# Kernel optimization log

Measured on AMD Instinct MI355X. Metric: run time of the kernel, lower is better.

Reference implementation:

```python
import jax, jax.numpy as jnp
import numpy as np

B, S, E, H = 4, 2048, 1024, 16
D = E // H


def setup_inputs() -> dict:
    key = jax.random.key(0)
    ks = jax.random.split(key, 8)
    inv = 1.0 / np.sqrt(E)
    return {
        "query": jax.random.normal(ks[0], (B, S, E), dtype=jnp.float32),
        "key": jax.random.normal(ks[1], (B, S, E), dtype=jnp.float32),
        "value": jax.random.normal(ks[2], (B, S, E), dtype=jnp.float32),
        "key_padding_mask": jnp.zeros((B, S), dtype=bool),
        "Wq": jax.random.uniform(ks[3], (E, E), jnp.float32, -inv, inv),
        "Wk": jax.random.uniform(ks[4], (E, E), jnp.float32, -inv, inv),
        "Wv": jax.random.uniform(ks[5], (E, E), jnp.float32, -inv, inv),
        "Wo": jax.random.uniform(ks[6], (E, E), jnp.float32, -inv, inv),
        "gamma": jnp.ones((H,), dtype=jnp.float32),
    }


def reference(query, key, value, key_padding_mask, Wq, Wk, Wv, Wo, gamma):
    b, s, e = query.shape
    h = gamma.shape[0]
    d = e // h
    # torch Linear: x @ W.T ; split into heads -> [b, h, s, d]
    q = (query @ Wq.T).reshape(b, s, h, d).swapaxes(1, 2)
    k = (key @ Wk.T).reshape(b, key.shape[1], h, d).swapaxes(1, 2)
    v = (value @ Wv.T).reshape(b, value.shape[1], h, d).swapaxes(1, 2)
    scores = jnp.einsum("bhqd,bhkd->bhqk", q, k) / jnp.sqrt(jnp.asarray(d, q.dtype))
    scores = jnp.where(key_padding_mask[:, None, None, :], -jnp.inf, scores)
    attn = jax.nn.softmax(scores, axis=-1)  # dropout p=0 in eval-equivalent reference
    out = jnp.einsum("bhqk,bhkd->bhqd", attn, v)
    out = out * gamma[None, :, None, None]  # head-scale
    out = out.swapaxes(1, 2).reshape(b, s, e)
    return out @ Wo.T
```

## Files before the change

kernel.cpp:

```cpp
#include <hip/hip_runtime.h>
#include <hip/hip_bf16.h>
#include <cstdint>

typedef __bf16 bf16;
typedef __bf16 bf16_8 __attribute__((ext_vector_type(8)));
typedef __bf16 bf16_4 __attribute__((ext_vector_type(4)));
typedef float f32_4 __attribute__((ext_vector_type(4)));
typedef short s16x4 __attribute__((ext_vector_type(4)));

#define MFMA_16x16x32(a, b, c) __builtin_amdgcn_mfma_f32_16x16x32_bf16((a), (b), (c), 0, 0, 0)
#define MFMA_16x16x16(a, b, c) __builtin_amdgcn_mfma_f32_16x16x16bf16_1k((a), (b), (c), 0, 0, 0)

__device__ __forceinline__ void gll16(const void* g, void* l) {
  __builtin_amdgcn_global_load_lds((const __attribute__((address_space(1))) void*)g,
                                   (__attribute__((address_space(3))) void*)l, 16, 0, 0);
}

__device__ __forceinline__ float exp2fast(float x) {
#if __has_builtin(__builtin_amdgcn_exp2f)
  return __builtin_amdgcn_exp2f(x);
#else
  return __exp2f(x);
#endif
}

__device__ __forceinline__ unsigned bfbits(float x) {
  bf16 b = (bf16)x;
  return (unsigned)__builtin_bit_cast(unsigned short, b);
}

__global__ __launch_bounds__(256) void cvt3(const float* __restrict__ s0,
                                            const float* __restrict__ s1,
                                            const float* __restrict__ s2,
                                            bf16* __restrict__ d0,
                                            bf16* __restrict__ d1,
                                            bf16* __restrict__ d2) {
  const float* srcs[3] = {s0, s1, s2};
  bf16* dsts[3] = {d0, d1, d2};
  const float* src = srcs[blockIdx.y];
  bf16* dst = dsts[blockIdx.y];
  size_t i = ((size_t)blockIdx.x * 256 + threadIdx.x) * 8;
  float4 f0 = *(const float4*)(src + i);
  float4 f1 = *(const float4*)(src + i + 4);
  bf16_8 v;
  v[0] = (bf16)f0.x; v[1] = (bf16)f0.y; v[2] = (bf16)f0.z; v[3] = (bf16)f0.w;
  v[4] = (bf16)f1.x; v[5] = (bf16)f1.y; v[6] = (bf16)f1.z; v[7] = (bf16)f1.w;
  *(bf16_8*)(dst + i) = v;
}

__global__ __launch_bounds__(256) void convert4(const float* __restrict__ w0,
                                                const float* __restrict__ w1,
                                                const float* __restrict__ w2,
                                                const float* __restrict__ w3,
                                                bf16* __restrict__ out, int per) {
  const float* srcs[4] = {w0, w1, w2, w3};
  const float* src = srcs[blockIdx.y];
  bf16* dst = out + (size_t)blockIdx.y * per;
  int i = (blockIdx.x * 256 + threadIdx.x) * 4;
  float4 f = *(const float4*)(src + i);
  bf16_4 v;
  v[0] = (bf16)f.x; v[1] = (bf16)f.y; v[2] = (bf16)f.z; v[3] = (bf16)f.w;
  *(bf16_4*)(dst + i) = v;
}

__global__ __launch_bounds__(256) void gemm_qkv(const bf16* __restrict__ Aq,
                                                const bf16* __restrict__ Ak,
                                                const bf16* __restrict__ Av,
                                                const bf16* __restrict__ W,
                                                bf16* __restrict__ Qp,
                                                bf16* __restrict__ Kp,
                                                bf16* __restrict__ Vt) {
  constexpr int BM = 128, BK = 32, K = 1024, N = 1024, M_S = 2048;
  __shared__ alignas(16) bf16 As[2][BM * BK];
  __shared__ alignas(16) bf16 Bs[2][BM * BK];

  const int tid = threadIdx.x;
  const int wave = tid >> 6, lane = tid & 63;
  const int quad = lane >> 4, l15 = lane & 15;
  const int wm = (wave & 1) * 64, wn = (wave >> 1) * 64;
  const int tensor = blockIdx.y >> 3;
  const int n0 = (blockIdx.y & 7) * 128;
  const size_t m0 = (size_t)blockIdx.x * BM;

  const bf16* A = tensor == 0 ? Aq : (tensor == 1 ? Ak : Av);
  const bf16* Bt = W + ((size_t)tensor << 20);

  f32_4 acc[4][4] = {};

  const size_t g_laneoff = (size_t)(lane >> 2) * K + (lane & 3) * 8;
  const bf16* Ag = A + (m0 + wave * 32) * (size_t)K + g_laneoff;
  const bf16* Bg = Bt + ((size_t)n0 + wave * 32) * (size_t)K + g_laneoff;
  const int l_off = wave * 32 * BK + lane * 8;

  auto stage = [&](int b, int k0) {
    gll16(Ag + k0, &As[b][l_off]);
    gll16(Ag + 16 * (size_t)K + k0, &As[b][l_off + 16 * BK]);
    gll16(Bg + k0, &Bs[b][l_off]);
    gll16(Bg + 16 * (size_t)K + k0, &Bs[b][l_off + 16 * BK]);
  };

  stage(0, 0);
  int buf = 0;
  for (int k0 = 0; k0 < K; k0 += BK, buf ^= 1) {
    __syncthreads();
    if (k0 + BK < K) stage(buf ^ 1, k0 + BK);

    bf16_8 af[4], bfr[4];
#pragma unroll
    for (int mt = 0; mt < 4; ++mt)
      af[mt] = *(const bf16_8*)&As[buf][(wm + mt * 16 + l15) * BK + quad * 8];
#pragma unroll
    for (int nt = 0; nt < 4; ++nt)
      bfr[nt] = *(const bf16_8*)&Bs[buf][(wn + nt * 16 + l15) * BK + quad * 8];
#pragma unroll
    for (int mt = 0; mt < 4; ++mt)
#pragma unroll
      for (int nt = 0; nt < 4; ++nt)
        acc[mt][nt] = MFMA_16x16x32(af[mt], bfr[nt], acc[mt][nt]);
  }

  if (tensor < 2) {
    bf16* C = tensor == 0 ? Qp : Kp;
#pragma unroll
    for (int mt = 0; mt < 4; ++mt)
#pragma unroll
      for (int i = 0; i < 4; ++i) {
        size_t row = m0 + wm + mt * 16 + quad * 4 + i;
        bf16* cr = C + row * N + n0 + wn + l15;
#pragma unroll
        for (int nt = 0; nt < 4; ++nt) cr[nt * 16] = (bf16)acc[mt][nt][i];
      }
  } else {
    const int bb = (int)(m0 >> 11);
    const int sbase = (int)(m0 & 2047) + wm;
#pragma unroll
    for (int mt = 0; mt < 4; ++mt)
#pragma unroll
      for (int nt = 0; nt < 4; ++nt) {
        int col = n0 + wn + nt * 16 + l15;
        bf16_4 pk;
        pk[0] = (bf16)acc[mt][nt][0]; pk[1] = (bf16)acc[mt][nt][1];
        pk[2] = (bf16)acc[mt][nt][2]; pk[3] = (bf16)acc[mt][nt][3];
        bf16* dst = Vt + ((size_t)(bb * 16 + (col >> 6)) * 64 + (col & 63)) * M_S +
                    sbase + mt * 16 + quad * 4;
        *(bf16_4*)dst = pk;
      }
  }
}

__global__ __launch_bounds__(256) void gemm_out(const bf16* __restrict__ A,
                                                const bf16* __restrict__ Bt,
                                                float* __restrict__ C,
                                                int M, int N, int K) {
  constexpr int BM = 128, BN = 128, BK = 32;
  __shared__ alignas(16) bf16 As[2][BM * BK];
  __shared__ alignas(16) bf16 Bs[2][BN * BK];

  const int tid = threadIdx.x;
  const int wave = tid >> 6, lane = tid & 63;
  const int quad = lane >> 4, l15 = lane & 15;
  const int wm = (wave & 1) * 64, wn = (wave >> 1) * 64;
  const size_t m0 = (size_t)blockIdx.x * BM;
  const size_t n0 = (size_t)blockIdx.y * BN;

  f32_4 acc[4][4] = {};

  const size_t g_laneoff = (size_t)(lane >> 2) * K + (lane & 3) * 8;
  const bf16* Ag = A + (m0 + wave * 32) * (size_t)K + g_laneoff;
  const bf16* Bg = Bt + (n0 + wave * 32) * (size_t)K + g_laneoff;
  const int l_off = wave * 32 * BK + lane * 8;

  auto stage = [&](int b, int k0) {
    gll16(Ag + k0, &As[b][l_off]);
    gll16(Ag + 16 * (size_t)K + k0, &As[b][l_off + 16 * BK]);
    gll16(Bg + k0, &Bs[b][l_off]);
    gll16(Bg + 16 * (size_t)K + k0, &Bs[b][l_off + 16 * BK]);
  };

  stage(0, 0);
  int buf = 0;
  for (int k0 = 0; k0 < K; k0 += BK, buf ^= 1) {
    __syncthreads();
    if (k0 + BK < K) stage(buf ^ 1, k0 + BK);

    bf16_8 af[4], bfr[4];
#pragma unroll
    for (int mt = 0; mt < 4; ++mt)
      af[mt] = *(const bf16_8*)&As[buf][(wm + mt * 16 + l15) * BK + quad * 8];
#pragma unroll
    for (int nt = 0; nt < 4; ++nt)
      bfr[nt] = *(const bf16_8*)&Bs[buf][(wn + nt * 16 + l15) * BK + quad * 8];
#pragma unroll
    for (int mt = 0; mt < 4; ++mt)
#pragma unroll
      for (int nt = 0; nt < 4; ++nt)
        acc[mt][nt] = MFMA_16x16x32(af[mt], bfr[nt], acc[mt][nt]);
  }

#pragma unroll
  for (int mt = 0; mt < 4; ++mt)
#pragma unroll
    for (int i = 0; i < 4; ++i) {
      size_t row = m0 + wm + mt * 16 + quad * 4 + i;
      float* cr = C + row * N + n0 + wn + l15;
#pragma unroll
      for (int nt = 0; nt < 4; ++nt) cr[nt * 16] = acc[mt][nt][i];
    }
}

__global__ __launch_bounds__(256, 3) void attn_fused(const bf16* __restrict__ Q,
                                                     const bf16* __restrict__ K,
                                                     const bf16* __restrict__ Vt,
                                                     const unsigned char* __restrict__ mask,
                                                     const float* __restrict__ gamma,
                                                     bf16* __restrict__ Out) {
  constexpr int S = 2048, E = 1024;
  constexpr float scale2 = 0.125f * 1.44269504f;
  constexpr float CB = -10.0f * 1.44269504f;
  constexpr float NEGB = -3.0e38f;
  __shared__ alignas(16) bf16 Ks[2][64 * 64];
  __shared__ alignas(16) bf16 Vs[2][64 * 64];

  const int tid = threadIdx.x;
  const int wave = tid >> 6, lane = tid & 63;
  const int quad = lane >> 4, l15 = lane & 15;
  const int q0 = blockIdx.x * 128;
  const int bh = blockIdx.y;
  const int b = bh >> 4, h = bh & 15;

  const int lrow = lane >> 3;
  const int sx = ((lane & 7) ^ lrow) * 8;
  const size_t koff = (size_t)lrow * E + sx;
  const size_t voff = (size_t)lrow * S + sx;

  const bf16* Qg = Q + ((size_t)(b * S + q0)) * E + h * 64;
  const bf16* Kg = K + ((size_t)b * S) * E + h * 64;
  const bf16* Vg = Vt + ((size_t)bh * 64) * S;
  const unsigned char* mg = mask + (size_t)b * S;

  auto stageKV = [&](int bf, int kt) {
#pragma unroll
    for (int p = 0; p < 2; ++p) {
      gll16(Kg + (size_t)(kt + wave * 16 + p * 8) * E + koff,
            &Ks[bf][(wave * 16 + p * 8) * 64 + lane * 8]);
      gll16(Vg + (size_t)(wave * 16 + p * 8) * S + voff + kt,
            &Vs[bf][(wave * 16 + p * 8) * 64 + lane * 8]);
    }
  };

  stageKV(0, 0);

  bf16_8 qf[2][2];
#pragma unroll
  for (int mt = 0; mt < 2; ++mt)
#pragma unroll
    for (int ks = 0; ks < 2; ++ks)
      qf[mt][ks] = *(const bf16_8*)(Qg + (size_t)(wave * 32 + mt * 16 + l15) * E +
                                    ks * 32 + quad * 8);

  f32_4 accO[4][2] = {};
  float rsum[2] = {};

  int buf = 0;
  for (int kt = 0; kt < S; kt += 64, buf ^= 1) {
    __syncthreads();
    if (kt + 64 < S) stageKV(buf ^ 1, kt + 64);

    f32_4 sT[4][2] = {};
#pragma unroll
    for (int ks = 0; ks < 2; ++ks)
#pragma unroll
      for (int t = 0; t < 4; ++t) {
        bf16_8 af = *(const bf16_8*)&Ks[buf][(t * 16 + l15) * 64 +
                                            (((ks * 4 + quad) ^ (l15 & 7)) * 8)];
        sT[t][0] = MFMA_16x16x32(af, qf[0][ks], sT[t][0]);
        sT[t][1] = MFMA_16x16x32(af, qf[1][ks], sT[t][1]);
      }

    s16x4 pk[4][2];
#pragma unroll
    for (int t = 0; t < 4; ++t) {
      const unsigned um = *(const unsigned*)(mg + kt + t * 16 + quad * 4);
      float bb[4];
#pragma unroll
      for (int i = 0; i < 4; ++i)
        bb[i] = ((um >> (8 * i)) & 0xffu) ? NEGB : CB;
#pragma unroll
      for (int mt = 0; mt < 2; ++mt) {
        float e0 = exp2fast(fmaf(sT[t][mt][0], scale2, bb[0]));
        float e1 = exp2fast(fmaf(sT[t][mt][1], scale2, bb[1]));
        float e2 = exp2fast(fmaf(sT[t][mt][2], scale2, bb[2]));
        float e3 = exp2fast(fmaf(sT[t][mt][3], scale2, bb[3]));
        rsum[mt] += (e0 + e1) + (e2 + e3);
        uint2 u;
        u.x = bfbits(e0) | (bfbits(e1) << 16);
        u.y = bfbits(e2) | (bfbits(e3) << 16);
        pk[t][mt] = __builtin_bit_cast(s16x4, u);
      }
    }

#pragma unroll
    for (int t = 0; t < 4; ++t)
#pragma unroll
      for (int dt = 0; dt < 4; ++dt) {
        const int chunk = (2 * t + (quad >> 1)) ^ (l15 & 7);
        s16x4 vf = *(const s16x4*)&Vs[buf][(dt * 16 + l15) * 64 + chunk * 8 +
                                           (quad & 1) * 4];
        accO[dt][0] = MFMA_16x16x16(vf, pk[t][0], accO[dt][0]);
        accO[dt][1] = MFMA_16x16x16(vf, pk[t][1], accO[dt][1]);
      }
  }

  const float g = gamma[h];
  float invv[2];
#pragma unroll
  for (int mt = 0; mt < 2; ++mt) {
    float s = rsum[mt];
    s += __shfl_xor(s, 16);
    s += __shfl_xor(s, 32);
    invv[mt] = g / s;
  }

#pragma unroll
  for (int mt = 0; mt < 2; ++mt) {
    size_t token = (size_t)(b * S) + q0 + wave * 32 + mt * 16 + l15;
    bf16* orow = Out + token * E + h * 64;
#pragma unroll
    for (int dt = 0; dt < 4; ++dt) {
      bf16_4 ov;
      ov[0] = (bf16)(accO[dt][mt][0] * invv[mt]);
      ov[1] = (bf16)(accO[dt][mt][1] * invv[mt]);
      ov[2] = (bf16)(accO[dt][mt][2] * invv[mt]);
      ov[3] = (bf16)(accO[dt][mt][3] * invv[mt]);
      *(bf16_4*)(orow + dt * 16 + quad * 4) = ov;
    }
  }
}

extern "C" void kernel_launch(void* const* d_in, const int* in_sizes, int n_in,
                              void* d_out, int out_size, void* d_ws, size_t ws_size,
                              hipStream_t stream) {
  constexpr int Bb = 4, S = 2048, E = 1024;
  constexpr int M = Bb * S;

  const float* q = (const float*)d_in[0];
  const float* k = (const float*)d_in[1];
  const float* v = (const float*)d_in[2];
  const unsigned char* mask = (const unsigned char*)d_in[3];
  const float* Wq = (const float*)d_in[4];
  const float* Wk = (const float*)d_in[5];
  const float* Wv = (const float*)d_in[6];
  const float* Wo = (const float*)d_in[7];
  const float* gamma = (const float*)d_in[8];

  char* ws = (char*)d_ws;
  bf16* Wb = (bf16*)ws;
  bf16* qb = (bf16*)(ws + ((size_t)8 << 20));
  bf16* kb = (bf16*)(ws + ((size_t)24 << 20));
  bf16* vb = (bf16*)(ws + ((size_t)40 << 20));
  bf16* Vt = (bf16*)(ws + ((size_t)56 << 20));
  bf16* Qp = (bf16*)d_out;
  bf16* Kp = (bf16*)d_out + ((size_t)1 << 23);

  convert4<<<dim3(1024, 4), 256, 0, stream>>>(Wq, Wk, Wv, Wo, Wb, 1 << 20);
  cvt3<<<dim3(4096, 3), 256, 0, stream>>>(q, k, v, qb, kb, vb);

  gemm_qkv<<<dim3(M / 128, 24), 256, 0, stream>>>(qb, kb, vb, Wb, Qp, Kp, Vt);

  bf16* At = qb;
  attn_fused<<<dim3(S / 128, Bb * 16), 256, 0, stream>>>(Qp, Kp, Vt, mask, gamma, At);

  gemm_out<<<dim3(M / 128, E / 128), 256, 0, stream>>>(At, Wb + (3 << 20), (float*)d_out, M, E, E);
}
```

Baseline: 354.8 us.

## Interleave Vt layout for 16-byte V loads, MFMA row sums, skip mask reads

The V-transpose store is permuted so that each lane can fetch one 16-byte LDS vector holding the two 4-element V fragments for adjacent key tiles, which halves the number of LDS reads in the PV loop. The softmax row sum now comes from an extra MFMA against a ones vector instead of VALU adds and cross-lane shuffles. A per-block pre-check detects whether the batch's padding mask has any set bits and skips the per-tile mask loads when it has none. Occupancy in the launch bounds rises from 3 to 4 blocks per CU, which may put pressure on registers. The row sum is now accumulated from the bf16-rounded probabilities, which slightly changes numerics.

```diff
diff --git a/kernel.cpp b/kernel.cpp
--- a/kernel.cpp
+++ b/kernel.cpp
@@ -7,6 +7,7 @@
 typedef __bf16 bf16_4 __attribute__((ext_vector_type(4)));
 typedef float f32_4 __attribute__((ext_vector_type(4)));
 typedef short s16x4 __attribute__((ext_vector_type(4)));
+typedef short s16x8 __attribute__((ext_vector_type(8)));
 
 #define MFMA_16x16x32(a, b, c) __builtin_amdgcn_mfma_f32_16x16x32_bf16((a), (b), (c), 0, 0, 0)
 #define MFMA_16x16x16(a, b, c) __builtin_amdgcn_mfma_f32_16x16x16bf16_1k((a), (b), (c), 0, 0, 0)
@@ -142,7 +143,7 @@
         pk[0] = (bf16)acc[mt][nt][0]; pk[1] = (bf16)acc[mt][nt][1];
         pk[2] = (bf16)acc[mt][nt][2]; pk[3] = (bf16)acc[mt][nt][3];
         bf16* dst = Vt + ((size_t)(bb * 16 + (col >> 6)) * 64 + (col & 63)) * M_S +
-                    sbase + mt * 16 + quad * 4;
+                    sbase + (mt >> 1) * 32 + quad * 8 + (mt & 1) * 4;
         *(bf16_4*)dst = pk;
       }
   }
@@ -208,7 +209,7 @@
     }
 }
 
-__global__ __launch_bounds__(256, 3) void attn_fused(const bf16* __restrict__ Q,
+__global__ __launch_bounds__(256, 4) void attn_fused(const bf16* __restrict__ Q,
                                                      const bf16* __restrict__ K,
                                                      const bf16* __restrict__ Vt,
                                                      const unsigned char* __restrict__ mask,
@@ -220,6 +221,7 @@
   constexpr float NEGB = -3.0e38f;
   __shared__ alignas(16) bf16 Ks[2][64 * 64];
   __shared__ alignas(16) bf16 Vs[2][64 * 64];
+  __shared__ int s_any;
 
   const int tid = threadIdx.x;
   const int wave = tid >> 6, lane = tid & 63;
@@ -228,6 +230,18 @@
   const int bh = blockIdx.y;
   const int b = bh >> 4, h = bh & 15;
 
+  const unsigned char* mg = mask + (size_t)b * S;
+
+  if (tid == 0) s_any = 0;
+  __syncthreads();
+  {
+    uint2 mv = ((const uint2*)mg)[tid];
+    unsigned long long bal = __ballot((mv.x | mv.y) != 0);
+    if (lane == 0 && bal) s_any = 1;
+  }
+  __syncthreads();
+  const bool anym = s_any != 0;
+
   const int lrow = lane >> 3;
   const int sx = ((lane & 7) ^ lrow) * 8;
   const size_t koff = (size_t)lrow * E + sx;
@@ -236,7 +250,6 @@
   const bf16* Qg = Q + ((size_t)(b * S + q0)) * E + h * 64;
   const bf16* Kg = K + ((size_t)b * S) * E + h * 64;
   const bf16* Vg = Vt + ((size_t)bh * 64) * S;
-  const unsigned char* mg = mask + (size_t)b * S;
 
   auto stageKV = [&](int bf, int kt) {
 #pragma unroll
@@ -258,8 +271,9 @@
       qf[mt][ks] = *(const bf16_8*)(Qg + (size_t)(wave * 32 + mt * 16 + l15) * E +
                                     ks * 32 + quad * 8);
 
+  const s16x4 onesA = {(short)0x3F80, (short)0x3F80, (short)0x3F80, (short)0x3F80};
   f32_4 accO[4][2] = {};
-  float rsum[2] = {};
+  f32_4 accR[2] = {};
 
   int buf = 0;
   for (int kt = 0; kt < S; kt += 64, buf ^= 1) {
@@ -280,46 +294,49 @@
     s16x4 pk[4][2];
 #pragma unroll
     for (int t = 0; t < 4; ++t) {
-      const unsigned um = *(const unsigned*)(mg + kt + t * 16 + quad * 4);
-      float bb[4];
-#pragma unroll
-      for (int i = 0; i < 4; ++i)
-        bb[i] = ((um >> (8 * i)) & 0xffu) ? NEGB : CB;
+      float bb0, bb1, bb2, bb3;
+      if (anym) {
+        const unsigned um = *(const unsigned*)(mg + kt + t * 16 + quad * 4);
+        bb0 = (um & 0xffu) ? NEGB : CB;
+        bb1 = (um & 0xff00u) ? NEGB : CB;
+        bb2 = (um & 0xff0000u) ? NEGB : CB;
+        bb3 = (um & 0xff000000u) ? NEGB : CB;
+      } else {
+        bb0 = bb1 = bb2 = bb3 = CB;
+      }
 #pragma unroll
       for (int mt = 0; mt < 2; ++mt) {
-        float e0 = exp2fast(fmaf(sT[t][mt][0], scale2, bb[0]));
-        float e1 = exp2fast(fmaf(sT[t][mt][1], scale2, bb[1]));
-        float e2 = exp2fast(fmaf(sT[t][mt][2], scale2, bb[2]));
-        float e3 = exp2fast(fmaf(sT[t][mt][3], scale2, bb[3]));
-        rsum[mt] += (e0 + e1) + (e2 + e3);
+        float e0 = exp2fast(fmaf(sT[t][mt][0], scale2, bb0));
+        float e1 = exp2fast(fmaf(sT[t][mt][1], scale2, bb1));
+        float e2 = exp2fast(fmaf(sT[t][mt][2], scale2, bb2));
+        float e3 = exp2fast(fmaf(sT[t][mt][3], scale2, bb3));
         uint2 u;
         u.x = bfbits(e0) | (bfbits(e1) << 16);
         u.y = bfbits(e2) | (bfbits(e3) << 16);
         pk[t][mt] = __builtin_bit_cast(s16x4, u);
+        accR[mt] = MFMA_16x16x16(onesA, pk[t][mt], accR[mt]);
       }
     }
 
 #pragma unroll
-    for (int t = 0; t < 4; ++t)
-#pragma unroll
-      for (int dt = 0; dt < 4; ++dt) {
-        const int chunk = (2 * t + (quad >> 1)) ^ (l15 & 7);
-        s16x4 vf = *(const s16x4*)&Vs[buf][(dt * 16 + l15) * 64 + chunk * 8 +
-                                           (quad & 1) * 4];
-        accO[dt][0] = MFMA_16x16x16(vf, pk[t][0], accO[dt][0]);
-        accO[dt][1] = MFMA_16x16x16(vf, pk[t][1], accO[dt][1]);
+    for (int dt = 0; dt < 4; ++dt)
+#pragma unroll
+      for (int i2 = 0; i2 < 2; ++i2) {
+        const int c = (i2 * 4 + quad) ^ (l15 & 7);
+        s16x8 w = *(const s16x8*)&Vs[buf][(dt * 16 + l15) * 64 + c * 8];
+        s16x4 lo = __builtin_shufflevector(w, w, 0, 1, 2, 3);
+        s16x4 hi = __builtin_shufflevector(w, w, 4, 5, 6, 7);
+        accO[dt][0] = MFMA_16x16x16(lo, pk[2 * i2][0], accO[dt][0]);
+        accO[dt][1] = MFMA_16x16x16(lo, pk[2 * i2][1], accO[dt][1]);
+        accO[dt][0] = MFMA_16x16x16(hi, pk[2 * i2 + 1][0], accO[dt][0]);
+        accO[dt][1] = MFMA_16x16x16(hi, pk[2 * i2 + 1][1], accO[dt][1]);
       }
   }
 
   const float g = gamma[h];
   float invv[2];
 #pragma unroll
-  for (int mt = 0; mt < 2; ++mt) {
-    float s = rsum[mt];
-    s += __shfl_xor(s, 16);
-    s += __shfl_xor(s, 32);
-    invv[mt] = g / s;
-  }
+  for (int mt = 0; mt < 2; ++mt) invv[mt] = g / accR[mt][0];
 
 #pragma unroll
   for (int mt = 0; mt < 2; ++mt) {
```

New measurement: 347.0 us. -2.2%, faster.
